# Kernel optimization log

Measured on AMD Instinct MI355X. Metric: run time of the kernel, lower is better.

Reference implementation:

```python
import jax, jax.numpy as jnp
import numpy as np

# Fixed deterministic sample of 8 offsets from the radius-4 ring (|dx|>1 or |dy|>1, not center).
# The torch module samples these randomly each step; we freeze them for reproducibility.
OFFSETS = [(-4, -4), (-4, -1), (-4, 2), (-3, 4), (-2, -3), (2, 3), (3, -2), (4, 4)]

B, C, H, W = 4, 16, 512, 512
DM, GH = 16, 32  # d_model, gating_hidden


def conv1x1(x, w, b):
    # 1x1 conv == per-pixel matmul: x [B,Cin,H,W], w [Cout,Cin], b [Cout]
    return jnp.einsum('bchw,dc->bdhw', x, w) + b[None, :, None, None]


def setup_inputs() -> dict:
    key = jax.random.key(0)
    ks = jax.random.split(key, 12)
    s_c = 1.0 / np.sqrt(C)
    s_2c = 1.0 / np.sqrt(2 * C)
    s_gh = 1.0 / np.sqrt(GH)
    return {
        'x': jax.random.normal(ks[0], (B, C, H, W), jnp.float32),
        'qw': jax.random.normal(ks[1], (DM, C), jnp.float32) * s_c,
        'qb': jnp.zeros((DM,), jnp.float32),
        'kw': jax.random.normal(ks[2], (DM, C), jnp.float32) * s_c,
        'kb': jnp.zeros((DM,), jnp.float32),
        'mw': jax.random.normal(ks[3], (C, C), jnp.float32) * s_c,
        'mb': jnp.zeros((C,), jnp.float32),
        'scaling': jnp.asarray(np.sqrt(DM), jnp.float32),
        'g1w': jax.random.normal(ks[4], (GH, 2 * C), jnp.float32) * s_2c,
        'g1b': jnp.zeros((GH,), jnp.float32),
        'g2w': jax.random.normal(ks[5], (C, GH), jnp.float32) * s_gh,
        'g2b': jnp.zeros((C,), jnp.float32),
    }


def reference(x, qw, qb, kw, kb, mw, mb, scaling, g1w, g1b, g2w, g2b):
    Q = conv1x1(x, qw, qb)            # [B,DM,H,W]
    K = conv1x1(x, kw, kb)            # [B,DM,H,W]
    M = conv1x1(x, mw, mb)            # [B,C,H,W]
    Q_pooled = Q.mean(axis=(2, 3))    # [B,DM]
    K_pooled = K.mean(axis=(2, 3))    # [B,DM]
    # torch.roll is circular, so the spatial mean of a rolled K equals K_pooled exactly;
    # every offset therefore produces the identical affinity (same math, cheaper).
    attn = (Q_pooled * K_pooled).sum(axis=1) / (scaling + 1e-6)   # [B]
    n = len(OFFSETS)
    # roll-based neighbor gather of messages: [n,B,C,H,W]
    msgs = jnp.stack([jnp.roll(M, (dy, dx), axis=(2, 3)) for dy, dx in OFFSETS], axis=0)
    affinities = jnp.broadcast_to(attn[None, :], (n, attn.shape[0]))  # [n,B]
    w = jax.nn.softmax(affinities, axis=0)[:, :, None, None, None]    # [n,B,1,1,1]
    agg = (msgs * w).sum(axis=0)                                      # [B,C,H,W]
    concat = jnp.concatenate([x, agg], axis=1)                        # [B,2C,H,W]
    hidden = jax.nn.relu(conv1x1(concat, g1w, g1b))                   # [B,GH,H,W]
    gate = jax.nn.sigmoid(conv1x1(hidden, g2w, g2b))                  # [B,C,H,W]
    return agg * gate
```

## Files before the change

### kernel.cpp

```cpp
#include <hip/hip_runtime.h>


#define HW 262144
#define WD 512

__global__ __launch_bounds__(256) void ga_fused(
    const float* __restrict__ x,
    const float* __restrict__ mw,  const float* __restrict__ mb,
    const float* __restrict__ g1w, const float* __restrict__ g1b,
    const float* __restrict__ g2w, const float* __restrict__ g2b,
    float* __restrict__ out)
{
  constexpr int DY[8] = {-4, -4, -4, -3, -2, 2, 3, 4};
  constexpr int DX[8] = {-4, -1,  2,  4, -3, 3, -2, 4};

  const int bh = blockIdx.x;
  const int b  = bh >> 9;
  const int h  = bh & 511;
  const int t  = threadIdx.x;
  const int w0 = t;
  const int w1 = t + 256;

  int roff[8], c0[8], c1[8];
#pragma unroll
  for (int i = 0; i < 8; ++i) {
    roff[i] = ((h - DY[i]) & 511) * WD;
    c0[i]   = (w0 - DX[i]) & 511;
    c1[i]   = (w1 - DX[i]) & 511;
  }

  const float* xb = x + b * 16 * HW;
  const int rowbase = h * WD;

  float xc0[16], xc1[16], xa0[16], xa1[16];
#pragma unroll
  for (int c = 0; c < 16; ++c) {
    const float* xp = xb + c * HW;
    xc0[c] = xp[rowbase + w0];
    xc1[c] = xp[rowbase + w1];
    float s0 = 0.f, s1 = 0.f;
#pragma unroll
    for (int i = 0; i < 8; ++i) {
      s0 += xp[roff[i] + c0[i]];
      s1 += xp[roff[i] + c1[i]];
    }
    xa0[c] = s0 * 0.125f;
    xa1[c] = s1 * 0.125f;
  }

  float ag0[16], ag1[16];
#pragma unroll
  for (int c = 0; c < 16; ++c) {
    float a0 = mb[c], a1 = mb[c];
#pragma unroll
    for (int k = 0; k < 16; ++k) {
      const float wv = mw[c * 16 + k];
      a0 = fmaf(wv, xa0[k], a0);
      a1 = fmaf(wv, xa1[k], a1);
    }
    ag0[c] = a0;
    ag1[c] = a1;
  }

  float hd0[32], hd1[32];
#pragma unroll
  for (int j = 0; j < 32; ++j) {
    float s0 = g1b[j], s1 = g1b[j];
#pragma unroll
    for (int k = 0; k < 16; ++k) {
      const float wx = g1w[j * 32 + k];
      const float wa = g1w[j * 32 + 16 + k];
      s0 = fmaf(wx, xc0[k], s0);
      s0 = fmaf(wa, ag0[k], s0);
      s1 = fmaf(wx, xc1[k], s1);
      s1 = fmaf(wa, ag1[k], s1);
    }
    hd0[j] = fmaxf(s0, 0.f);
    hd1[j] = fmaxf(s1, 0.f);
  }

  float* ob = out + b * 16 * HW + rowbase;
#pragma unroll
  for (int c = 0; c < 16; ++c) {
    float s0 = g2b[c], s1 = g2b[c];
#pragma unroll
    for (int j = 0; j < 32; ++j) {
      const float wv = g2w[c * 32 + j];
      s0 = fmaf(wv, hd0[j], s0);
      s1 = fmaf(wv, hd1[j], s1);
    }
    const float gt0 = 1.0f / (1.0f + __expf(-s0));
    const float gt1 = 1.0f / (1.0f + __expf(-s1));
    ob[c * HW + w0] = ag0[c] * gt0;
    ob[c * HW + w1] = ag1[c] * gt1;
  }
}

extern "C" void kernel_launch(void* const* d_in, const int* in_sizes, int n_in,
                              void* d_out, int out_size, void* d_ws, size_t ws_size,
                              hipStream_t stream) {
  const float* x   = (const float*)d_in[0];
  const float* mw  = (const float*)d_in[5];
  const float* mb  = (const float*)d_in[6];
  const float* g1w = (const float*)d_in[8];
  const float* g1b = (const float*)d_in[9];
  const float* g2w = (const float*)d_in[10];
  const float* g2b = (const float*)d_in[11];
  float* out = (float*)d_out;

  ga_fused<<<2048, 256, 0, stream>>>(x, mw, mb, g1w, g1b, g2w, g2b, out);
}
```

Baseline: 193.5 us.

## Vectorize gathers and stores with float2, remap blocks to half-rows with swizzle

Each thread now handles two adjacent pixels, so the center load, the five even-dx neighbor loads and the output store become float2 accesses. The three odd-dx offsets stay as scalar loads. Blocks shrink to 128 threads covering half a row, and a swizzled block index interleaves rows to change L2 locality. The goal is fewer memory instructions and better cache reuse of the stencil gathers. In exchange, the neighbor address arithmetic gets more complex, and the misaligned odd offsets still need two scalar loads each.

```diff
diff --git a/kernel.cpp b/kernel.cpp
--- a/kernel.cpp
+++ b/kernel.cpp
@@ -4,7 +4,7 @@
 #define HW 262144
 #define WD 512
 
-__global__ __launch_bounds__(256) void ga_fused(
+__global__ __launch_bounds__(128) void ga_fused(
     const float* __restrict__ x,
     const float* __restrict__ mw,  const float* __restrict__ mb,
     const float* __restrict__ g1w, const float* __restrict__ g1b,
@@ -14,35 +14,54 @@
   constexpr int DY[8] = {-4, -4, -4, -3, -2, 2, 3, 4};
   constexpr int DX[8] = {-4, -1,  2,  4, -3, 3, -2, 4};
 
-  const int bh = blockIdx.x;
-  const int b  = bh >> 9;
-  const int h  = bh & 511;
-  const int t  = threadIdx.x;
-  const int w0 = t;
-  const int w1 = t + 256;
-
-  int roff[8], c0[8], c1[8];
-#pragma unroll
-  for (int i = 0; i < 8; ++i) {
-    roff[i] = ((h - DY[i]) & 511) * WD;
-    c0[i]   = (w0 - DX[i]) & 511;
-    c1[i]   = (w1 - DX[i]) & 511;
-  }
+  const int bid = blockIdx.x;
+  const int sw  = ((bid & 7) << 9) + (bid >> 3);
+  const int b    = sw >> 10;
+  const int r    = (sw >> 1) & 511;
+  const int half = sw & 1;
+  const int t    = threadIdx.x;
+  const int w0   = (half << 8) + (t << 1);
 
   const float* xb = x + b * 16 * HW;
-  const int rowbase = h * WD;
+  const int rowbase = r * WD;
+
+  unsigned eoff[5];
+  unsigned o0[3], o1[3];
+  {
+    const int EI[5] = {0, 2, 3, 6, 7};
+#pragma unroll
+    for (int k = 0; k < 5; ++k) {
+      const int i = EI[k];
+      eoff[k] = ((r - DY[i]) & 511) * WD + ((w0 - DX[i]) & 511);
+    }
+    const int OI[3] = {1, 4, 5};
+#pragma unroll
+    for (int k = 0; k < 3; ++k) {
+      const int i = OI[k];
+      const unsigned ro = ((r - DY[i]) & 511) * WD;
+      o0[k] = ro + ((w0     - DX[i]) & 511);
+      o1[k] = ro + ((w0 + 1 - DX[i]) & 511);
+    }
+  }
 
   float xc0[16], xc1[16], xa0[16], xa1[16];
 #pragma unroll
   for (int c = 0; c < 16; ++c) {
     const float* xp = xb + c * HW;
-    xc0[c] = xp[rowbase + w0];
-    xc1[c] = xp[rowbase + w1];
+    const float2 ctr = *reinterpret_cast<const float2*>(xp + rowbase + w0);
+    xc0[c] = ctr.x;
+    xc1[c] = ctr.y;
     float s0 = 0.f, s1 = 0.f;
 #pragma unroll
-    for (int i = 0; i < 8; ++i) {
-      s0 += xp[roff[i] + c0[i]];
-      s1 += xp[roff[i] + c1[i]];
+    for (int k = 0; k < 5; ++k) {
+      const float2 v = *reinterpret_cast<const float2*>(xp + eoff[k]);
+      s0 += v.x;
+      s1 += v.y;
+    }
+#pragma unroll
+    for (int k = 0; k < 3; ++k) {
+      s0 += xp[o0[k]];
+      s1 += xp[o1[k]];
     }
     xa0[c] = s0 * 0.125f;
     xa1[c] = s1 * 0.125f;
@@ -91,8 +110,10 @@
     }
     const float gt0 = 1.0f / (1.0f + __expf(-s0));
     const float gt1 = 1.0f / (1.0f + __expf(-s1));
-    ob[c * HW + w0] = ag0[c] * gt0;
-    ob[c * HW + w1] = ag1[c] * gt1;
+    float2 o;
+    o.x = ag0[c] * gt0;
+    o.y = ag1[c] * gt1;
+    *reinterpret_cast<float2*>(ob + c * HW + w0) = o;
   }
 }
 
@@ -108,5 +129,5 @@
   const float* g2b = (const float*)d_in[11];
   float* out = (float*)d_out;
 
-  ga_fused<<<2048, 256, 0, stream>>>(x, mw, mb, g1w, g1b, g2w, g2b, out);
+  ga_fused<<<4096, 128, 0, stream>>>(x, mw, mb, g1w, g1b, g2w, g2b, out);
 }
```

Measured after the change: 213.9 us. 1.11x slower.

## Use one pixel per thread, stream matmul accumulation, and swizzle block order

Applied to the files above, without the earlier changes.

Each thread now handles one pixel instead of two, and the grid doubles to 4096 blocks. The message matmul and the two gating layers are accumulated on the fly, so the hidden array is never held in registers. This cuts register pressure, and the launch bounds ask for 8 waves per SIMD to raise occupancy. A block-index swizzle spreads neighbouring rows across XCDs for L2 locality, at the cost of fewer independent FMA chains per thread.

```diff
diff --git a/kernel.cpp b/kernel.cpp
--- a/kernel.cpp
+++ b/kernel.cpp
@@ -4,7 +4,7 @@
 #define HW 262144
 #define WD 512
 
-__global__ __launch_bounds__(256) void ga_fused(
+__global__ __launch_bounds__(256, 8) void ga_fused(
     const float* __restrict__ x,
     const float* __restrict__ mw,  const float* __restrict__ mb,
     const float* __restrict__ g1w, const float* __restrict__ g1b,
@@ -14,85 +14,61 @@
   constexpr int DY[8] = {-4, -4, -4, -3, -2, 2, 3, 4};
   constexpr int DX[8] = {-4, -1,  2,  4, -3, 3, -2, 4};
 
-  const int bh = blockIdx.x;
-  const int b  = bh >> 9;
-  const int h  = bh & 511;
-  const int t  = threadIdx.x;
-  const int w0 = t;
-  const int w1 = t + 256;
-
-  int roff[8], c0[8], c1[8];
-#pragma unroll
-  for (int i = 0; i < 8; ++i) {
-    roff[i] = ((h - DY[i]) & 511) * WD;
-    c0[i]   = (w0 - DX[i]) & 511;
-    c1[i]   = (w1 - DX[i]) & 511;
-  }
+  const int bid = blockIdx.x;
+  const int sw  = ((bid & 7) << 9) + (bid >> 3);
+  const int b    = sw >> 10;
+  const int r    = (sw >> 1) & 511;
+  const int half = sw & 1;
+  const int w    = (half << 8) + threadIdx.x;
 
   const float* xb = x + b * 16 * HW;
-  const int rowbase = h * WD;
+  const int rowbase = r * WD;
 
-  float xc0[16], xc1[16], xa0[16], xa1[16];
+  unsigned off[8];
+#pragma unroll
+  for (int i = 0; i < 8; ++i)
+    off[i] = ((r - DY[i]) & 511) * WD + ((w - DX[i]) & 511);
+
+  float xc[16], ag[16];
+#pragma unroll
+  for (int cc = 0; cc < 16; ++cc) ag[cc] = mb[cc];
+
 #pragma unroll
   for (int c = 0; c < 16; ++c) {
     const float* xp = xb + c * HW;
-    xc0[c] = xp[rowbase + w0];
-    xc1[c] = xp[rowbase + w1];
-    float s0 = 0.f, s1 = 0.f;
+    xc[c] = xp[rowbase + w];
+    float s = 0.f;
 #pragma unroll
-    for (int i = 0; i < 8; ++i) {
-      s0 += xp[roff[i] + c0[i]];
-      s1 += xp[roff[i] + c1[i]];
-    }
-    xa0[c] = s0 * 0.125f;
-    xa1[c] = s1 * 0.125f;
+    for (int i = 0; i < 8; ++i) s += xp[off[i]];
+    const float xa = s * 0.125f;
+#pragma unroll
+    for (int cc = 0; cc < 16; ++cc)
+      ag[cc] = fmaf(mw[cc * 16 + c], xa, ag[cc]);
   }
 
-  float ag0[16], ag1[16];
+  float sg[16];
+#pragma unroll
+  for (int c = 0; c < 16; ++c) sg[c] = g2b[c];
+
+#pragma unroll
+  for (int j = 0; j < 32; ++j) {
+    float s = g1b[j];
+#pragma unroll
+    for (int k = 0; k < 16; ++k) {
+      s = fmaf(g1w[j * 32 + k],      xc[k], s);
+      s = fmaf(g1w[j * 32 + 16 + k], ag[k], s);
+    }
+    const float hd = fmaxf(s, 0.f);
+#pragma unroll
+    for (int c = 0; c < 16; ++c)
+      sg[c] = fmaf(g2w[c * 32 + j], hd, sg[c]);
+  }
+
+  float* ob = out + b * 16 * HW + rowbase + w;
 #pragma unroll
   for (int c = 0; c < 16; ++c) {
-    float a0 = mb[c], a1 = mb[c];
-#pragma unroll
-    for (int k = 0; k < 16; ++k) {
-      const float wv = mw[c * 16 + k];
-      a0 = fmaf(wv, xa0[k], a0);
-      a1 = fmaf(wv, xa1[k], a1);
-    }
-    ag0[c] = a0;
-    ag1[c] = a1;
-  }
-
-  float hd0[32], hd1[32];
-#pragma unroll
-  for (int j = 0; j < 32; ++j) {
-    float s0 = g1b[j], s1 = g1b[j];
-#pragma unroll
-    for (int k = 0; k < 16; ++k) {
-      const float wx = g1w[j * 32 + k];
-      const float wa = g1w[j * 32 + 16 + k];
-      s0 = fmaf(wx, xc0[k], s0);
-      s0 = fmaf(wa, ag0[k], s0);
-      s1 = fmaf(wx, xc1[k], s1);
-      s1 = fmaf(wa, ag1[k], s1);
-    }
-    hd0[j] = fmaxf(s0, 0.f);
-    hd1[j] = fmaxf(s1, 0.f);
-  }
-
-  float* ob = out + b * 16 * HW + rowbase;
-#pragma unroll
-  for (int c = 0; c < 16; ++c) {
-    float s0 = g2b[c], s1 = g2b[c];
-#pragma unroll
-    for (int j = 0; j < 32; ++j) {
-      const float wv = g2w[c * 32 + j];
-      s0 = fmaf(wv, hd0[j], s0);
-      s1 = fmaf(wv, hd1[j], s1);
-    }
-    const float gt0 = 1.0f / (1.0f + __expf(-s0));
-    const float gt1 = 1.0f / (1.0f + __expf(-s1));
-    ob[c * HW + w0] = ag0[c] * gt0;
-    ob[c * HW + w1] = ag1[c] * gt1;
+    const float gt = 1.0f / (1.0f + __expf(-sg[c]));
+    ob[c * HW] = ag[c] * gt;
   }
 }
 
@@ -108,5 +84,5 @@
   const float* g2b = (const float*)d_in[11];
   float* out = (float*)d_out;
 
-  ga_fused<<<2048, 256, 0, stream>>>(x, mw, mb, g1w, g1b, g2w, g2b, out);
+  ga_fused<<<4096, 256, 0, stream>>>(x, mw, mb, g1w, g1b, g2w, g2b, out);
 }
```

Result: slower. 478.0 us (+147.1%).
